# Kernel tuning notes

Hardware: AMD Instinct MI355X
Metric: run time of the kernel (lower is better)

The kernel has to match this reference:

```python
import jax, jax.numpy as jnp
import numpy as np

N, E, IN, HID, H, OUT = 50000, 800000, 128, 64, 4, 128
NEG = 0.2   # LeakyReLU slope in GATv2
EPS = 1e-5  # BatchNorm eps


def _seg_softmax(a, seg, n):
    # numerically stable softmax over edges grouped by destination node
    amax = jax.lax.stop_gradient(jax.ops.segment_max(a, seg, num_segments=n))
    amax = jnp.where(jnp.isfinite(amax), amax, 0.0)
    ex = jnp.exp(a - amax[seg])
    den = jax.ops.segment_sum(ex, seg, num_segments=n)
    return ex / (den[seg] + 1e-16)


def _gatv2(x, src, dst, e_attr, Wl, bl, Wr, br, We, att, bias, heads, c, concat):
    n = x.shape[0]
    xl = (x @ Wl + bl).reshape(n, heads, c)   # source transform (x_j)
    xr = (x @ Wr + br).reshape(n, heads, c)   # target transform (x_i)
    ee = (e_attr @ We).reshape(-1, heads, c)  # edge feature transform
    m = xl[src] + xr[dst] + ee                # [E, H, C]
    m = jnp.where(m > 0, m, NEG * m)          # LeakyReLU
    alpha = _seg_softmax(jnp.einsum('ehc,hc->eh', m, att), dst, n)  # [E, H]
    out = jax.ops.segment_sum(alpha[:, :, None] * xl[src], dst, num_segments=n)
    out = out.reshape(n, heads * c) if concat else out.mean(axis=1)
    return out + bias


def _bn(h, g, b):  # BatchNorm1d, training-mode batch stats (biased var)
    mu = jnp.mean(h, axis=0)
    var = jnp.var(h, axis=0)
    return (h - mu) * jax.lax.rsqrt(var + EPS) * g + b


def _prelu(h, a):
    return jnp.where(h > 0, h, a * h)


def setup_inputs() -> dict:
    key = jax.random.key(0)
    ks = jax.random.split(key, 16)
    def nrm(k, shape, fan):
        return jax.random.normal(k, shape, jnp.float32) / np.float32(np.sqrt(fan))
    x = jax.random.normal(ks[0], (N, IN), jnp.float32)
    edge_index = jax.random.randint(ks[1], (2, E), 0, N, jnp.int32)
    edge_attr = jax.random.uniform(ks[2], (E, 1), dtype=jnp.float32)
    return {
        'x': x, 'edge_index': edge_index, 'edge_attr': edge_attr,
        # layer 1: heads=4, concat=True
        'Wl1': nrm(ks[3], (IN, H * HID), IN), 'bl1': jnp.zeros((H * HID,), jnp.float32),
        'Wr1': nrm(ks[4], (IN, H * HID), IN), 'br1': jnp.zeros((H * HID,), jnp.float32),
        'We1': nrm(ks[5], (1, H * HID), 1),
        'att1': nrm(ks[6], (H, HID), HID),
        'cb1': jnp.zeros((H * HID,), jnp.float32),
        'bng1': jnp.ones((H * HID,), jnp.float32), 'bnb1': jnp.zeros((H * HID,), jnp.float32),
        'pa': jnp.float32(0.25),  # PReLU single parameter (shared by both uses)
        # layer 2: heads=1, concat=False
        'Wl2': nrm(ks[7], (H * HID, OUT), H * HID), 'bl2': jnp.zeros((OUT,), jnp.float32),
        'Wr2': nrm(ks[8], (H * HID, OUT), H * HID), 'br2': jnp.zeros((OUT,), jnp.float32),
        'We2': nrm(ks[9], (1, OUT), 1),
        'att2': nrm(ks[10], (1, OUT), OUT),
        'cb2': jnp.zeros((OUT,), jnp.float32),
        'bng2': jnp.ones((OUT,), jnp.float32), 'bnb2': jnp.zeros((OUT,), jnp.float32),
        'skipW': nrm(ks[11], (IN, OUT), IN), 'skipb': jnp.zeros((OUT,), jnp.float32),
    }


def reference(x, edge_index, edge_attr, Wl1, bl1, Wr1, br1, We1, att1, cb1,
              bng1, bnb1, pa, Wl2, bl2, Wr2, br2, We2, att2, cb2, bng2, bnb2,
              skipW, skipb):
    src, dst = edge_index[0], edge_index[1]
    h = _gatv2(x, src, dst, edge_attr, Wl1, bl1, Wr1, br1, We1, att1, cb1, H, HID, True)
    h = _prelu(_bn(h, bng1, bnb1), pa)  # dropout = identity (eval)
    h = _gatv2(h, src, dst, edge_attr, Wl2, bl2, Wr2, br2, We2, att2, cb2, 1, OUT, False)
    h = _prelu(_bn(h, bng2, bnb2), pa)
    return h + (x @ skipW + skipb)
```

## Files before the change

### kernel.cpp

```cpp
#include <hip/hip_runtime.h>
#include <cstdint>
#include <cstddef>

#define NNODES 50000
#define NEDGES 800000
#define DH1    256
#define DOUT   128

#define K1F 0.8656170245333781f
#define K2F 0.5770780163555854f

typedef unsigned short u16;
typedef __bf16 bf16x8 __attribute__((ext_vector_type(8)));
typedef float  f32x4  __attribute__((ext_vector_type(4)));

__device__ __forceinline__ float bf2f(unsigned int u) {
  union { unsigned int i; float f; } x; x.i = u << 16; return x.f;
}
__device__ __forceinline__ u16 f2bf(float f) {
  union { float f; unsigned int i; } x; x.f = f;
  unsigned int r = x.i + 0x7fffu + ((x.i >> 16) & 1u);
  return (u16)(r >> 16);
}
__device__ __forceinline__ void dec8(uint4 r, float* o) {
  o[0] = bf2f(r.x & 0xffffu); o[1] = bf2f(r.x >> 16);
  o[2] = bf2f(r.y & 0xffffu); o[3] = bf2f(r.y >> 16);
  o[4] = bf2f(r.z & 0xffffu); o[5] = bf2f(r.z >> 16);
  o[6] = bf2f(r.w & 0xffffu); o[7] = bf2f(r.w >> 16);
}
__device__ __forceinline__ uint4 pack8(const float* v) {
  uint4 p;
  p.x = (unsigned)f2bf(v[0]) | ((unsigned)f2bf(v[1]) << 16);
  p.y = (unsigned)f2bf(v[2]) | ((unsigned)f2bf(v[3]) << 16);
  p.z = (unsigned)f2bf(v[4]) | ((unsigned)f2bf(v[5]) << 16);
  p.w = (unsigned)f2bf(v[6]) | ((unsigned)f2bf(v[7]) << 16);
  return p;
}
template<int CTRL>
__device__ __forceinline__ float dppadd(float v) {
  int t = __builtin_amdgcn_update_dpp(0, __float_as_int(v), CTRL, 0xF, 0xF, true);
  return v + __int_as_float(t);
}
__device__ __forceinline__ float fexp2(float x) {
#if __has_builtin(__builtin_amdgcn_exp2f)
  return __builtin_amdgcn_exp2f(x);
#else
  return exp2f(x);
#endif
}


#define CNT_BLKS 3125
#define CVT_BLKS 6250
#define W1_BLKS  320
#define W2_BLKS  256

__global__ __launch_bounds__(256) void setup_k(
    const int* __restrict__ dst, int* __restrict__ cnt, int* __restrict__ rank,
    const float* __restrict__ x, u16* __restrict__ xbf,
    const float* __restrict__ Wl1, const float* __restrict__ Wr1,
    const float* __restrict__ bl1, const float* __restrict__ br1,
    const float* __restrict__ Wl2, const float* __restrict__ Wr2,
    const float* __restrict__ bl2, const float* __restrict__ br2,
    const float* __restrict__ skW, const float* __restrict__ skb,
    const float* __restrict__ att1, const float* __restrict__ We1,
    const float* __restrict__ att2, const float* __restrict__ We2,
    u16* __restrict__ Wcat1, float* __restrict__ bias1,
    u16* __restrict__ Wt2, float* __restrict__ bias2,
    float* __restrict__ axw, int2* __restrict__ epair) {
  int b = blockIdx.x, t = threadIdx.x;
  if (b < CNT_BLKS) {
    int e = b * 256 + t;
    if (e < NEDGES) rank[e] = atomicAdd(&cnt[dst[e]], 1);
  } else if (b < CNT_BLKS + CVT_BLKS) {
    int i = ((b - CNT_BLKS) * 256 + t) * 4;
    float4 v = *reinterpret_cast<const float4*>(x + i);
    uint2 pk;
    pk.x = (unsigned)f2bf(v.x) | ((unsigned)f2bf(v.y) << 16);
    pk.y = (unsigned)f2bf(v.z) | ((unsigned)f2bf(v.w) << 16);
    *reinterpret_cast<uint2*>(xbf + i) = pk;
  } else if (b < CNT_BLKS + CVT_BLKS + W1_BLKS) {
    int idx = (b - CNT_BLKS - CVT_BLKS) * 256 + t;
    if (idx < 640) bias1[idx] = idx < 256 ? bl1[idx] : idx < 512 ? br1[idx - 256] : skb[idx - 512];
    int n = idx >> 7, k = idx & 127;
    float v = n < 256 ? Wl1[k * 256 + n] : n < 512 ? Wr1[k * 256 + (n - 256)] : skW[k * 128 + (n - 512)];
    Wcat1[idx] = f2bf(v);
  } else if (b < CNT_BLKS + CVT_BLKS + W1_BLKS + W2_BLKS) {
    int idx = (b - CNT_BLKS - CVT_BLKS - W1_BLKS) * 256 + t;
    if (idx < 256) bias2[idx] = idx < 128 ? bl2[idx] : br2[idx - 128];
    int n = idx >> 8, k = idx & 255;
    float v = n < 128 ? Wl2[k * 128 + n] : Wr2[k * 128 + (n - 128)];
    Wt2[idx] = f2bf(v);
  } else if (b == CNT_BLKS + CVT_BLKS + W1_BLKS + W2_BLKS) {
    if (t < 4) {
      float s = 0.f;
      for (int c = 0; c < 64; ++c) s += att1[t * 64 + c] * We1[t * 64 + c];
      axw[t] = s * K1F;
    } else if (t == 4) {
      float s = 0.f;
      for (int c = 0; c < 128; ++c) s += att2[c] * We2[c];
      axw[4] = s * K1F;
    }
  } else {
    int2 z; z.x = 0; z.y = 0;
    epair[NEDGES + t] = z;
  }
}


__global__ __launch_bounds__(256) void offsets_k(const int* __restrict__ cnt, int* __restrict__ offs,
                                                 int* __restrict__ total) {
  int i = blockIdx.x * 256 + threadIdx.x;
  int lane = threadIdx.x & 63;
  int c = (i < NNODES) ? cnt[i] : 0;
  int incl = c;
  #pragma unroll
  for (int d = 1; d < 64; d <<= 1) {
    int t = __shfl_up(incl, d, 64);
    if (lane >= d) incl += t;
  }
  int wtotal = __shfl(incl, 63, 64);
  int base = 0;
  if (lane == 63) base = atomicAdd(total, wtotal);
  base = __shfl(base, 63, 64);
  int off = base + incl - c;
  if (i < NNODES) offs[i] = off;
}

__global__ __launch_bounds__(256) void scatter_k(const int* __restrict__ src, const int* __restrict__ dst,
                                                 const float* __restrict__ ea, const int* __restrict__ offs,
                                                 const int* __restrict__ rank, int2* __restrict__ epair) {
  int e = blockIdx.x * 256 + threadIdx.x;
  if (e >= NEDGES) return;
  int p = offs[dst[e]] + rank[e];
  int2 v; v.x = src[e]; v.y = __float_as_int(ea[e]);
  epair[p] = v;
}


template<int K, int NPASS, int B1, int B2, int LDC0, int LDC1, int LDC2,
         int SPAN, int ATTLEN, bool DO_ATT, bool FUSE_BN>
__global__ __launch_bounds__(512) void gemm_fused(
    const u16* __restrict__ A, const u16* __restrict__ Wt, const float* __restrict__ bias,
    u16* __restrict__ C0, u16* __restrict__ C1, u16* __restrict__ C2,
    const float* __restrict__ att, float* __restrict__ axl, float* __restrict__ axr,
    const float* __restrict__ bnsum, const float* __restrict__ bnsq,
    const float* __restrict__ bng, const float* __restrict__ bnb,
    const float* __restrict__ pap) {
  constexpr int LDA = K + 8;
  constexpr int CSTR = 136;
  __shared__ __align__(16) u16 As[64 * LDA];
  __shared__ __align__(16) u16 Cs[64 * CSTR];
  __shared__ float attS[128];
  __shared__ float scS[K], shS[K];
  const int tid = threadIdx.x;
  const int row0 = blockIdx.x * 64;

  if constexpr (FUSE_BN) {
    if (tid < K) {
      const float invN = 1.0f / (float)NNODES;
      float mu = bnsum[tid] * invN;
      float var = bnsq[tid] * invN - mu * mu;
      float s = bng[tid] * rsqrtf(var + 1e-5f);
      scS[tid] = s;
      shS[tid] = bnb[tid] - mu * s;
    }
    __syncthreads();
  }
  const float pa = FUSE_BN ? pap[0] : 0.f;
  #pragma unroll
  for (int it = 0; it < K / 32; ++it) {
    int chunk = it * 512 + tid;
    int row = chunk / (K / 4);
    int col = (chunk % (K / 4)) * 4;
    uint2 v; v.x = 0u; v.y = 0u;
    int gr = row0 + row;
    if (gr < NNODES) v = *reinterpret_cast<const uint2*>(A + (size_t)gr * K + col);
    if constexpr (FUSE_BN) {
      float o0 = bf2f(v.x & 0xffffu) * scS[col]     + shS[col];
      float o1 = bf2f(v.x >> 16)     * scS[col + 1] + shS[col + 1];
      float o2 = bf2f(v.y & 0xffffu) * scS[col + 2] + shS[col + 2];
      float o3 = bf2f(v.y >> 16)     * scS[col + 3] + shS[col + 3];
      o0 = o0 > 0.f ? o0 : pa * o0;
      o1 = o1 > 0.f ? o1 : pa * o1;
      o2 = o2 > 0.f ? o2 : pa * o2;
      o3 = o3 > 0.f ? o3 : pa * o3;
      v.x = (unsigned)f2bf(o0) | ((unsigned)f2bf(o1) << 16);
      v.y = (unsigned)f2bf(o2) | ((unsigned)f2bf(o3) << 16);
    }
    *reinterpret_cast<uint2*>(&As[row * LDA + col]) = v;
  }
  __syncthreads();

  const int w = tid >> 6, lane = tid & 63, q = lane >> 4, l16 = lane & 15;
  const int tc = w * 16 + l16;

  #pragma unroll
  for (int p = 0; p < NPASS; ++p) {
    const int cb = p * 128;
    const int ncol = cb + tc;
    f32x4 acc[4];
    #pragma unroll
    for (int rt = 0; rt < 4; ++rt) acc[rt] = (f32x4){0.f, 0.f, 0.f, 0.f};
    const u16* wp = Wt + (size_t)ncol * K + q * 8;
    #pragma unroll
    for (int ks = 0; ks < K / 32; ++ks) {
      bf16x8 b = *reinterpret_cast<const bf16x8*>(wp + ks * 32);
      #pragma unroll
      for (int rt = 0; rt < 4; ++rt) {
        bf16x8 a = *reinterpret_cast<const bf16x8*>(&As[(rt * 16 + l16) * LDA + ks * 32 + q * 8]);
        acc[rt] = __builtin_amdgcn_mfma_f32_16x16x32_bf16(a, b, acc[rt], 0, 0, 0);
      }
    }
    const float bval = bias[ncol];
    #pragma unroll
    for (int rt = 0; rt < 4; ++rt)
      #pragma unroll
      for (int r = 0; r < 4; ++r)
        Cs[(rt * 16 + q * 4 + r) * CSTR + tc] = f2bf(acc[rt][r] + bval);
    if (DO_ATT && cb < B2 && tid < 128) attS[tid] = att[(cb + tid) % ATTLEN];
    __syncthreads();
    {
      u16* Cg; int LD, cc;
      if (cb < B1)      { Cg = C0; LD = LDC0; cc = cb; }
      else if (cb < B2) { Cg = C1; LD = LDC1; cc = cb - B1; }
      else              { Cg = C2; LD = LDC2; cc = cb - B2; }
      #pragma unroll
      for (int it = 0; it < 2; ++it) {
        int ch = it * 512 + tid;
        int row = ch / 16, co = (ch % 16) * 8;
        int grow = row0 + row;
        if (grow < NNODES) {
          uint4 v = *reinterpret_cast<const uint4*>(&Cs[row * CSTR + co]);
          *reinterpret_cast<uint4*>(Cg + (size_t)grow * LD + cc + co) = v;
        }
      }
    }
    if constexpr (DO_ATT) {
      if (cb < B2) {
        constexpr int TPU = SPAN / 16;
        constexpr int HIT = 128 / SPAN;
        constexpr int HEADS = B1 / SPAN;
        int unit = tid / TPU, sub = tid % TPU;
        int row = unit / HIT, hb = unit % HIT;
        int c0 = hb * SPAN + sub * 16;
        float s = 0.f;
        #pragma unroll
        for (int c = 0; c < 16; ++c)
          s += bf2f(Cs[row * CSTR + c0 + c]) * attS[c0 + c];
        #pragma unroll
        for (int d = 1; d < TPU; d <<= 1) s += __shfl_xor(s, d, 64);
        int grow = row0 + row;
        if (sub == 0 && grow < NNODES) {
          int cbl = cb < B1 ? cb : cb - B1;
          int head = cbl / SPAN + hb;
          float* dstp = (cb < B1) ? axl : axr;
          dstp[grow * HEADS + head] = s * K1F;
        }
      }
    }
    __syncthreads();
  }
}


template<int HEADS, int CHAN, int EPW>
__global__ __launch_bounds__(256) void gat_edge(
    const int* __restrict__ offs, const int* __restrict__ cnt,
    const int2* __restrict__ epair,
    const u16* __restrict__ xl, const u16* __restrict__ xr,
    const float* __restrict__ att, const float* __restrict__ We,
    const float* __restrict__ cb,
    const float* __restrict__ axl, const float* __restrict__ axr,
    const float* __restrict__ aWep, u16* __restrict__ hout) {
  constexpr int HC  = HEADS * CHAN;
  constexpr int GSZ = 64 / EPW;
  constexpr int CPL = HC / GSZ;
  constexpr int LPH = CHAN / CPL;
  static_assert(CPL == 8, "layout");

  int node = __builtin_amdgcn_readfirstlane((int)(blockIdx.x * 4 + (threadIdx.x >> 6)));
  if (node >= NNODES) return;
  const int lane = threadIdx.x & 63;
  const int g    = lane / GSZ;
  const int lgs  = lane & (GSZ - 1);
  const int h    = lgs / LPH;
  const int cbase = lgs * CPL;

  float xrv[8], attv[8], wev[8];
  {
    uint4 xrr = *reinterpret_cast<const uint4*>(xr + (size_t)node * HC + cbase);
    dec8(xrr, xrv);
    float4 a0 = *reinterpret_cast<const float4*>(att + cbase);
    float4 a1 = *reinterpret_cast<const float4*>(att + cbase + 4);
    float4 w0 = *reinterpret_cast<const float4*>(We + cbase);
    float4 w1 = *reinterpret_cast<const float4*>(We + cbase + 4);
    attv[0]=a0.x*K2F; attv[1]=a0.y*K2F; attv[2]=a0.z*K2F; attv[3]=a0.w*K2F;
    attv[4]=a1.x*K2F; attv[5]=a1.y*K2F; attv[6]=a1.z*K2F; attv[7]=a1.w*K2F;
    wev[0]=w0.x; wev[1]=w0.y; wev[2]=w0.z; wev[3]=w0.w;
    wev[4]=w1.x; wev[5]=w1.y; wev[6]=w1.z; wev[7]=w1.w;
  }
  const float aWe = aWep[h];
  const float axr_n = axr[node * HEADS + h];
  const int off = __builtin_amdgcn_readfirstlane(offs[node]);
  const int deg = __builtin_amdgcn_readfirstlane(cnt[node]);

  const char* __restrict__ xlb  = (const char*)xl;
  const char* __restrict__ axlb = (const char*)axl;
  const unsigned cboff = (unsigned)(cbase * 2);
  const unsigned hoff  = (unsigned)(h * 4);

  float den = 0.f;
  float accv[8];
  #pragma unroll
  for (int c = 0; c < 8; ++c) accv[c] = 0.f;

  const int niter = (deg + EPW - 1) / EPW;
  const int2* pp = epair + off + g;
  int2 p0 = pp[0];
  int2 p1 = pp[EPW];
  int2 p2 = pp[2 * EPW];
  uint4 r0, r1; float ax0, ax1;
  {
    unsigned b0 = (unsigned)p0.x * (unsigned)(HC * 2) + cboff;
    r0  = *reinterpret_cast<const uint4*>(xlb + b0);
    ax0 = *reinterpret_cast<const float*>(axlb + ((unsigned)p0.x * (unsigned)(HEADS * 4) + hoff));
    unsigned b1 = (unsigned)p1.x * (unsigned)(HC * 2) + cboff;
    r1  = *reinterpret_cast<const uint4*>(xlb + b1);
    ax1 = *reinterpret_cast<const float*>(axlb + ((unsigned)p1.x * (unsigned)(HEADS * 4) + hoff));
  }
  const int lastg = deg - 1 - (niter - 1) * EPW;
  for (int i = 0; i < niter; ++i) {
    int2 p3 = pp[(i + 3) * EPW];
    uint4 r2; float ax2;
    {
      unsigned b2 = (unsigned)p2.x * (unsigned)(HC * 2) + cboff;
      r2  = *reinterpret_cast<const uint4*>(xlb + b2);
      ax2 = *reinterpret_cast<const float*>(axlb + ((unsigned)p2.x * (unsigned)(HEADS * 4) + hoff));
    }
    float ea = __int_as_float(p0.y);
    float xlv[8];
    dec8(r0, xlv);
    float part2 = 0.f;
    #pragma unroll
    for (int c = 0; c < 8; ++c) {
      float m = xlv[c] + fmaf(ea, wev[c], xrv[c]);
      part2 = fmaf(fabsf(m), attv[c], part2);
    }
    if constexpr (LPH >= 2)  part2 = dppadd<0xB1>(part2);
    if constexpr (LPH >= 4)  part2 = dppadd<0x4E>(part2);
    if constexpr (LPH >= 8)  part2 = dppadd<0x141>(part2);
    if constexpr (LPH >= 16) part2 = dppadd<0x140>(part2);
    float e = fexp2(part2 + fmaf(ea, aWe, axr_n) + ax0);
    if (i == niter - 1) e = (g <= lastg) ? e : 0.f;
    den += e;
    #pragma unroll
    for (int c = 0; c < 8; ++c) accv[c] = fmaf(e, xlv[c], accv[c]);
    p0 = p1; p1 = p2; p2 = p3; r0 = r1; r1 = r2; ax0 = ax1; ax1 = ax2;
  }
  #pragma unroll
  for (int d = GSZ; d < 64; d <<= 1) {
    den += __shfl_xor(den, d, 64);
    #pragma unroll
    for (int c = 0; c < 8; ++c) accv[c] += __shfl_xor(accv[c], d, 64);
  }
  if (g == 0) {
    float inv = 1.0f / (den + 1e-16f);
    float4 c0 = *reinterpret_cast<const float4*>(cb + cbase);
    float4 c1 = *reinterpret_cast<const float4*>(cb + cbase + 4);
    float ov[8];
    ov[0] = accv[0] * inv + c0.x; ov[1] = accv[1] * inv + c0.y;
    ov[2] = accv[2] * inv + c0.z; ov[3] = accv[3] * inv + c0.w;
    ov[4] = accv[4] * inv + c1.x; ov[5] = accv[5] * inv + c1.y;
    ov[6] = accv[6] * inv + c1.z; ov[7] = accv[7] * inv + c1.w;
    *reinterpret_cast<uint4*>(hout + (size_t)node * HC + cbase) = pack8(ov);
  }
}


template<int NC>
__global__ void bn_stats_bf(const u16* __restrict__ h, float* __restrict__ sum, float* __restrict__ sq) {
  int c = threadIdx.x;
  float s = 0.f, q = 0.f;
  for (int r = blockIdx.x; r < NNODES; r += gridDim.x) {
    float v = bf2f(h[(size_t)r * NC + c]);
    s += v; q += v * v;
  }
  atomicAdd(&sum[c], s);
  atomicAdd(&sq[c], q);
}

__global__ __launch_bounds__(256) void final_out_k(
    const u16* __restrict__ h2, const u16* __restrict__ skip,
    const float* __restrict__ sum, const float* __restrict__ sq,
    const float* __restrict__ g, const float* __restrict__ bb_,
    const float* __restrict__ pap, float* __restrict__ outp, int total) {
  int i = (blockIdx.x * 256 + threadIdx.x) * 4;
  if (i >= total) return;
  const float invN = 1.0f / (float)NNODES;
  float pa = pap[0];
  int c = i & 127;
  float4 sm = *reinterpret_cast<const float4*>(sum + c);
  float4 qq = *reinterpret_cast<const float4*>(sq + c);
  float4 gg = *reinterpret_cast<const float4*>(g + c);
  float4 bb = *reinterpret_cast<const float4*>(bb_ + c);
  float mu, var, sc[4], sh[4];
  mu = sm.x * invN; var = qq.x * invN - mu * mu; sc[0] = gg.x * rsqrtf(var + 1e-5f); sh[0] = bb.x - mu * sc[0];
  mu = sm.y * invN; var = qq.y * invN - mu * mu; sc[1] = gg.y * rsqrtf(var + 1e-5f); sh[1] = bb.y - mu * sc[1];
  mu = sm.z * invN; var = qq.z * invN - mu * mu; sc[2] = gg.z * rsqrtf(var + 1e-5f); sh[2] = bb.z - mu * sc[2];
  mu = sm.w * invN; var = qq.w * invN - mu * mu; sc[3] = gg.w * rsqrtf(var + 1e-5f); sh[3] = bb.w - mu * sc[3];
  uint2 raw = *reinterpret_cast<const uint2*>(h2 + i);
  float v0 = bf2f(raw.x & 0xffffu), v1 = bf2f(raw.x >> 16);
  float v2 = bf2f(raw.y & 0xffffu), v3 = bf2f(raw.y >> 16);
  uint2 skr = *reinterpret_cast<const uint2*>(skip + i);
  float s0 = bf2f(skr.x & 0xffffu), s1 = bf2f(skr.x >> 16);
  float s2 = bf2f(skr.y & 0xffffu), s3 = bf2f(skr.y >> 16);
  float4 o;
  o.x = v0 * sc[0] + sh[0]; o.x = (o.x > 0.f ? o.x : pa * o.x) + s0;
  o.y = v1 * sc[1] + sh[1]; o.y = (o.y > 0.f ? o.y : pa * o.y) + s1;
  o.z = v2 * sc[2] + sh[2]; o.z = (o.z > 0.f ? o.z : pa * o.z) + s2;
  o.w = v3 * sc[3] + sh[3]; o.w = (o.w > 0.f ? o.w : pa * o.w) + s3;
  *reinterpret_cast<float4*>(outp + i) = o;
}


extern "C" void kernel_launch(void* const* d_in, const int* in_sizes, int n_in,
                              void* d_out, int out_size, void* d_ws, size_t ws_size,
                              hipStream_t stream) {
  (void)in_sizes; (void)n_in; (void)out_size; (void)ws_size;
  const float* x    = (const float*)d_in[0];
  const int*   ei   = (const int*)d_in[1];
  const float* ea   = (const float*)d_in[2];
  const float* Wl1  = (const float*)d_in[3];
  const float* bl1  = (const float*)d_in[4];
  const float* Wr1  = (const float*)d_in[5];
  const float* br1  = (const float*)d_in[6];
  const float* We1  = (const float*)d_in[7];
  const float* att1 = (const float*)d_in[8];
  const float* cb1  = (const float*)d_in[9];
  const float* bng1 = (const float*)d_in[10];
  const float* bnb1 = (const float*)d_in[11];
  const float* pa   = (const float*)d_in[12];
  const float* Wl2  = (const float*)d_in[13];
  const float* bl2  = (const float*)d_in[14];
  const float* Wr2  = (const float*)d_in[15];
  const float* br2  = (const float*)d_in[16];
  const float* We2  = (const float*)d_in[17];
  const float* att2 = (const float*)d_in[18];
  const float* cb2  = (const float*)d_in[19];
  const float* bng2 = (const float*)d_in[20];
  const float* bnb2 = (const float*)d_in[21];
  const float* skW  = (const float*)d_in[22];
  const float* skb  = (const float*)d_in[23];
  const int* srcp = ei;
  const int* dstp = ei + NEDGES;

  char* base = (char*)d_ws;
  size_t off = 0;
  auto alloc = [&](size_t bytes) -> char* {
    char* p = base + off;
    off = (off + bytes + 255) & ~(size_t)255;
    return p;
  };
  size_t zero_ints = 1 + NNODES + 256 + 256 + 128 + 128;
  char* zbase = alloc(zero_ints * 4);
  int*   totalp = (int*)zbase;
  int*   cnt    = totalp + 1;
  float* bnsum1 = (float*)(cnt + NNODES);
  float* bnsq1  = bnsum1 + 256;
  float* bnsum2 = bnsq1 + 256;
  float* bnsq2  = bnsum2 + 128;

  int*   offs    = (int*)alloc((size_t)NNODES * 4);
  int*   rank    = (int*)alloc((size_t)NEDGES * 4);
  int2*  epair   = (int2*)alloc(((size_t)NEDGES + 256) * 8);
  const size_t RBYTES = (size_t)NNODES * DH1 * 2;
  char* regionA = alloc(RBYTES);
  char* regionB = alloc(RBYTES);
  char* regionC = alloc(RBYTES);
  u16*   xbf    = (u16*)alloc((size_t)NNODES * 128 * 2);
  u16*   skipbf = (u16*)alloc((size_t)NNODES * 128 * 2);
  u16*   Wcat1  = (u16*)alloc(640 * 128 * 2);
  u16*   Wt2    = (u16*)alloc(256 * 256 * 2);
  float* bias1  = (float*)alloc(640 * 4);
  float* bias2  = (float*)alloc(256 * 4);
  float* axw    = (float*)alloc(8 * 4);
  float* axl1   = (float*)alloc((size_t)NNODES * 4 * 4);
  float* axr1   = (float*)alloc((size_t)NNODES * 4 * 4);
  float* axl2   = (float*)alloc((size_t)NNODES * 4);
  float* axr2   = (float*)alloc((size_t)NNODES * 4);

  u16*   xl1     = (u16*)regionA;
  u16*   xr1     = (u16*)regionB;
  u16*   h1      = (u16*)regionC;
  u16*   xl2     = (u16*)regionB;
  u16*   xr2     = (u16*)(regionB + (size_t)NNODES * DOUT * 2);
  u16*   h2      = (u16*)regionA;

  hipMemsetAsync(zbase, 0, zero_ints * 4, stream);

  const int EB = (NEDGES + 255) / 256;
  const int NB = (NNODES + 255) / 256;
  setup_k<<<CNT_BLKS + CVT_BLKS + W1_BLKS + W2_BLKS + 2, 256, 0, stream>>>(
      dstp, cnt, rank, x, xbf, Wl1, Wr1, bl1, br1, Wl2, Wr2, bl2, br2, skW, skb,
      att1, We1, att2, We2, Wcat1, bias1, Wt2, bias2, axw, epair);
  offsets_k<<<NB, 256, 0, stream>>>(cnt, offs, totalp);
  scatter_k<<<EB, 256, 0, stream>>>(srcp, dstp, ea, offs, rank, epair);

  const int MB64 = (NNODES + 63) / 64;
  gemm_fused<128, 5, 256, 512, 256, 256, 128, 64, 256, true, false><<<MB64, 512, 0, stream>>>(
      xbf, Wcat1, bias1, xl1, xr1, skipbf, att1, axl1, axr1,
      (const float*)0, (const float*)0, (const float*)0, (const float*)0, (const float*)0);
  gat_edge<4, 64, 2><<<(NNODES + 3) / 4, 256, 0, stream>>>(
      offs, cnt, epair, xl1, xr1, att1, We1, cb1, axl1, axr1, axw, h1);
  bn_stats_bf<256><<<800, 256, 0, stream>>>(h1, bnsum1, bnsq1);

  gemm_fused<256, 2, 128, 256, 128, 128, 1, 128, 128, true, true><<<MB64, 512, 0, stream>>>(
      h1, Wt2, bias2, xl2, xr2, (u16*)0, att2, axl2, axr2,
      bnsum1, bnsq1, bng1, bnb1, pa);
  gat_edge<1, 128, 4><<<(NNODES + 3) / 4, 256, 0, stream>>>(
      offs, cnt, epair, xl2, xr2, att2, We2, cb2, axl2, axr2, axw + 4, h2);
  bn_stats_bf<128><<<800, 128, 0, stream>>>(h2, bnsum2, bnsq2);
  final_out_k<<<(NNODES * DOUT / 4 + 255) / 256, 256, 0, stream>>>(
      h2, skipbf, bnsum2, bnsq2, bng2, bnb2, pa, (float*)d_out, NNODES * DOUT);
}
```

Measured before the change: 439.5 us.

## Make GAT edge kernels persistent with per-partition atomic node work queues

Replaces the one-wave-per-node launch of the GAT edge aggregation kernels with a fixed grid of 2048 blocks. Each wave repeatedly claims the next node from one of 64 node partitions through an atomic counter and processes it. The software prefetch depth is reduced from three edges ahead to two, and the tail mask is now applied on every iteration. The intent is to balance the uneven per-node degrees, cut launch and wave startup overhead, and keep nearby nodes on the same blocks for cache locality. In exchange it adds an atomic per node, and the shallower prefetch may expose more gather latency.

```diff
diff --git a/kernel.cpp b/kernel.cpp
--- a/kernel.cpp
+++ b/kernel.cpp
@@ -6,6 +6,10 @@
 #define NEDGES 800000
 #define DH1    256
 #define DOUT   128
+
+#define NPART  64
+#define PSZ    782
+#define GATBLK 2048
 
 #define K1F 0.8656170245333781f
 #define K2F 0.5770780163555854f
@@ -272,25 +276,22 @@
     const float* __restrict__ att, const float* __restrict__ We,
     const float* __restrict__ cb,
     const float* __restrict__ axl, const float* __restrict__ axr,
-    const float* __restrict__ aWep, u16* __restrict__ hout) {
+    const float* __restrict__ aWep, u16* __restrict__ hout,
+    int* __restrict__ ctr) {
   constexpr int HC  = HEADS * CHAN;
   constexpr int GSZ = 64 / EPW;
   constexpr int CPL = HC / GSZ;
   constexpr int LPH = CHAN / CPL;
   static_assert(CPL == 8, "layout");
 
-  int node = __builtin_amdgcn_readfirstlane((int)(blockIdx.x * 4 + (threadIdx.x >> 6)));
-  if (node >= NNODES) return;
   const int lane = threadIdx.x & 63;
   const int g    = lane / GSZ;
   const int lgs  = lane & (GSZ - 1);
   const int h    = lgs / LPH;
   const int cbase = lgs * CPL;
 
-  float xrv[8], attv[8], wev[8];
+  float attv[8], wev[8];
   {
-    uint4 xrr = *reinterpret_cast<const uint4*>(xr + (size_t)node * HC + cbase);
-    dec8(xrr, xrv);
     float4 a0 = *reinterpret_cast<const float4*>(att + cbase);
     float4 a1 = *reinterpret_cast<const float4*>(att + cbase + 4);
     float4 w0 = *reinterpret_cast<const float4*>(We + cbase);
@@ -301,79 +302,91 @@
     wev[4]=w1.x; wev[5]=w1.y; wev[6]=w1.z; wev[7]=w1.w;
   }
   const float aWe = aWep[h];
-  const float axr_n = axr[node * HEADS + h];
-  const int off = __builtin_amdgcn_readfirstlane(offs[node]);
-  const int deg = __builtin_amdgcn_readfirstlane(cnt[node]);
+
+  const int part  = blockIdx.x & (NPART - 1);
+  const int pbase = part * PSZ;
+  const int pcnt  = (NNODES - pbase) < PSZ ? (NNODES - pbase) : PSZ;
+  int* ctrp = ctr + part;
 
   const char* __restrict__ xlb  = (const char*)xl;
   const char* __restrict__ axlb = (const char*)axl;
   const unsigned cboff = (unsigned)(cbase * 2);
   const unsigned hoff  = (unsigned)(h * 4);
 
-  float den = 0.f;
-  float accv[8];
-  #pragma unroll
-  for (int c = 0; c < 8; ++c) accv[c] = 0.f;
-
-  const int niter = (deg + EPW - 1) / EPW;
-  const int2* pp = epair + off + g;
-  int2 p0 = pp[0];
-  int2 p1 = pp[EPW];
-  int2 p2 = pp[2 * EPW];
-  uint4 r0, r1; float ax0, ax1;
-  {
-    unsigned b0 = (unsigned)p0.x * (unsigned)(HC * 2) + cboff;
-    r0  = *reinterpret_cast<const uint4*>(xlb + b0);
-    ax0 = *reinterpret_cast<const float*>(axlb + ((unsigned)p0.x * (unsigned)(HEADS * 4) + hoff));
-    unsigned b1 = (unsigned)p1.x * (unsigned)(HC * 2) + cboff;
-    r1  = *reinterpret_cast<const uint4*>(xlb + b1);
-    ax1 = *reinterpret_cast<const float*>(axlb + ((unsigned)p1.x * (unsigned)(HEADS * 4) + hoff));
-  }
-  const int lastg = deg - 1 - (niter - 1) * EPW;
-  for (int i = 0; i < niter; ++i) {
-    int2 p3 = pp[(i + 3) * EPW];
-    uint4 r2; float ax2;
+  for (;;) {
+    int myn = 0;
+    if (lane == 0) myn = atomicAdd(ctrp, 1);
+    myn = __shfl(myn, 0, 64);
+    if (myn >= pcnt) break;
+    const int node = __builtin_amdgcn_readfirstlane(pbase + myn);
+
+    float xrv[8];
+    dec8(*reinterpret_cast<const uint4*>(xr + (size_t)node * HC + cbase), xrv);
+    const float axr_n = axr[node * HEADS + h];
+    const int off = __builtin_amdgcn_readfirstlane(offs[node]);
+    const int deg = __builtin_amdgcn_readfirstlane(cnt[node]);
+    const int limg = deg - g;
+
+    float den = 0.f;
+    float accv[8];
+    #pragma unroll
+    for (int c = 0; c < 8; ++c) accv[c] = 0.f;
+
+    const int niter = (deg + EPW - 1) / EPW;
+    const int2* pp = epair + off + g;
+    int2 p_cur = pp[0];
+    int2 p_nxt = pp[EPW];
+    uint4 r_cur; float ax_cur;
     {
-      unsigned b2 = (unsigned)p2.x * (unsigned)(HC * 2) + cboff;
-      r2  = *reinterpret_cast<const uint4*>(xlb + b2);
-      ax2 = *reinterpret_cast<const float*>(axlb + ((unsigned)p2.x * (unsigned)(HEADS * 4) + hoff));
-    }
-    float ea = __int_as_float(p0.y);
-    float xlv[8];
-    dec8(r0, xlv);
-    float part2 = 0.f;
+      unsigned b0 = (unsigned)p_cur.x * (unsigned)(HC * 2) + cboff;
+      r_cur  = *reinterpret_cast<const uint4*>(xlb + b0);
+      ax_cur = *reinterpret_cast<const float*>(axlb + ((unsigned)p_cur.x * (unsigned)(HEADS * 4) + hoff));
+    }
+    for (int i = 0; i < niter; ++i) {
+      int2 p_n2 = pp[(i + 2) * EPW];
+      uint4 r_n; float ax_n;
+      {
+        unsigned b1 = (unsigned)p_nxt.x * (unsigned)(HC * 2) + cboff;
+        r_n  = *reinterpret_cast<const uint4*>(xlb + b1);
+        ax_n = *reinterpret_cast<const float*>(axlb + ((unsigned)p_nxt.x * (unsigned)(HEADS * 4) + hoff));
+      }
+      float ea = __int_as_float(p_cur.y);
+      float xlv[8];
+      dec8(r_cur, xlv);
+      float part2 = 0.f;
+      #pragma unroll
+      for (int c = 0; c < 8; ++c) {
+        float m = xlv[c] + fmaf(ea, wev[c], xrv[c]);
+        part2 = fmaf(fabsf(m), attv[c], part2);
+      }
+      if constexpr (LPH >= 2)  part2 = dppadd<0xB1>(part2);
+      if constexpr (LPH >= 4)  part2 = dppadd<0x4E>(part2);
+      if constexpr (LPH >= 8)  part2 = dppadd<0x141>(part2);
+      if constexpr (LPH >= 16) part2 = dppadd<0x140>(part2);
+      float e = fexp2(part2 + fmaf(ea, aWe, axr_n) + ax_cur);
+      e = (i * EPW < limg) ? e : 0.f;
+      den += e;
+      #pragma unroll
+      for (int c = 0; c < 8; ++c) accv[c] = fmaf(e, xlv[c], accv[c]);
+      p_cur = p_nxt; p_nxt = p_n2; r_cur = r_n; ax_cur = ax_n;
+    }
     #pragma unroll
-    for (int c = 0; c < 8; ++c) {
-      float m = xlv[c] + fmaf(ea, wev[c], xrv[c]);
-      part2 = fmaf(fabsf(m), attv[c], part2);
-    }
-    if constexpr (LPH >= 2)  part2 = dppadd<0xB1>(part2);
-    if constexpr (LPH >= 4)  part2 = dppadd<0x4E>(part2);
-    if constexpr (LPH >= 8)  part2 = dppadd<0x141>(part2);
-    if constexpr (LPH >= 16) part2 = dppadd<0x140>(part2);
-    float e = fexp2(part2 + fmaf(ea, aWe, axr_n) + ax0);
-    if (i == niter - 1) e = (g <= lastg) ? e : 0.f;
-    den += e;
-    #pragma unroll
-    for (int c = 0; c < 8; ++c) accv[c] = fmaf(e, xlv[c], accv[c]);
-    p0 = p1; p1 = p2; p2 = p3; r0 = r1; r1 = r2; ax0 = ax1; ax1 = ax2;
-  }
-  #pragma unroll
-  for (int d = GSZ; d < 64; d <<= 1) {
-    den += __shfl_xor(den, d, 64);
-    #pragma unroll
-    for (int c = 0; c < 8; ++c) accv[c] += __shfl_xor(accv[c], d, 64);
-  }
-  if (g == 0) {
-    float inv = 1.0f / (den + 1e-16f);
-    float4 c0 = *reinterpret_cast<const float4*>(cb + cbase);
-    float4 c1 = *reinterpret_cast<const float4*>(cb + cbase + 4);
-    float ov[8];
-    ov[0] = accv[0] * inv + c0.x; ov[1] = accv[1] * inv + c0.y;
-    ov[2] = accv[2] * inv + c0.z; ov[3] = accv[3] * inv + c0.w;
-    ov[4] = accv[4] * inv + c1.x; ov[5] = accv[5] * inv + c1.y;
-    ov[6] = accv[6] * inv + c1.z; ov[7] = accv[7] * inv + c1.w;
-    *reinterpret_cast<uint4*>(hout + (size_t)node * HC + cbase) = pack8(ov);
+    for (int d = GSZ; d < 64; d <<= 1) {
+      den += __shfl_xor(den, d, 64);
+      #pragma unroll
+      for (int c = 0; c < 8; ++c) accv[c] += __shfl_xor(accv[c], d, 64);
+    }
+    if (g == 0) {
+      float inv = 1.0f / (den + 1e-16f);
+      float4 c0 = *reinterpret_cast<const float4*>(cb + cbase);
+      float4 c1 = *reinterpret_cast<const float4*>(cb + cbase + 4);
+      float ov[8];
+      ov[0] = accv[0] * inv + c0.x; ov[1] = accv[1] * inv + c0.y;
+      ov[2] = accv[2] * inv + c0.z; ov[3] = accv[3] * inv + c0.w;
+      ov[4] = accv[4] * inv + c1.x; ov[5] = accv[5] * inv + c1.y;
+      ov[6] = accv[6] * inv + c1.z; ov[7] = accv[7] * inv + c1.w;
+      *reinterpret_cast<uint4*>(hout + (size_t)node * HC + cbase) = pack8(ov);
+    }
   }
 }
 
@@ -462,7 +475,7 @@
     off = (off + bytes + 255) & ~(size_t)255;
     return p;
   };
-  size_t zero_ints = 1 + NNODES + 256 + 256 + 128 + 128;
+  size_t zero_ints = 1 + NNODES + 256 + 256 + 128 + 128 + 2 * NPART;
   char* zbase = alloc(zero_ints * 4);
   int*   totalp = (int*)zbase;
   int*   cnt    = totalp + 1;
@@ -470,6 +483,8 @@
   float* bnsq1  = bnsum1 + 256;
   float* bnsum2 = bnsq1 + 256;
   float* bnsq2  = bnsum2 + 128;
+  int*   ctr1   = (int*)(bnsq2 + 128);
+  int*   ctr2   = ctr1 + NPART;
 
   int*   offs    = (int*)alloc((size_t)NNODES * 4);
   int*   rank    = (int*)alloc((size_t)NEDGES * 4);
@@ -511,15 +526,15 @@
   gemm_fused<128, 5, 256, 512, 256, 256, 128, 64, 256, true, false><<<MB64, 512, 0, stream>>>(
       xbf, Wcat1, bias1, xl1, xr1, skipbf, att1, axl1, axr1,
       (const float*)0, (const float*)0, (const float*)0, (const float*)0, (const float*)0);
-  gat_edge<4, 64, 2><<<(NNODES + 3) / 4, 256, 0, stream>>>(
-      offs, cnt, epair, xl1, xr1, att1, We1, cb1, axl1, axr1, axw, h1);
+  gat_edge<4, 64, 2><<<GATBLK, 256, 0, stream>>>(
+      offs, cnt, epair, xl1, xr1, att1, We1, cb1, axl1, axr1, axw, h1, ctr1);
   bn_stats_bf<256><<<800, 256, 0, stream>>>(h1, bnsum1, bnsq1);
 
   gemm_fused<256, 2, 128, 256, 128, 128, 1, 128, 128, true, true><<<MB64, 512, 0, stream>>>(
       h1, Wt2, bias2, xl2, xr2, (u16*)0, att2, axl2, axr2,
       bnsum1, bnsq1, bng1, bnb1, pa);
-  gat_edge<1, 128, 4><<<(NNODES + 3) / 4, 256, 0, stream>>>(
-      offs, cnt, epair, xl2, xr2, att2, We2, cb2, axl2, axr2, axw + 4, h2);
+  gat_edge<1, 128, 4><<<GATBLK, 256, 0, stream>>>(
+      offs, cnt, epair, xl2, xr2, att2, We2, cb2, axl2, axr2, axw + 4, h2, ctr2);
   bn_stats_bf<128><<<800, 128, 0, stream>>>(h2, bnsum2, bnsq2);
   final_out_k<<<(NNODES * DOUT / 4 + 255) / 256, 256, 0, stream>>>(
       h2, skipbf, bnsum2, bnsq2, bng2, bnb2, pa, (float*)d_out, NNODES * DOUT);
```

Result: slower. 773.1 us (+75.9%).

## Split layer-1 edge aggregation per head and shorten gather prefetch depth

Applied to the files above, without the earlier changes.

The layer-1 GAT edge kernel now gives each wavefront a single (node, head) pair. Each wave handles 8 edges at a time with 8 lanes per 64-channel head, where before one wave covered all four heads at 2 edges per pass. Block indices are interleaved so the four head-blocks of a node group launch close together, which should let them share the gathered source rows in cache. The software prefetch pipeline is also cut from two edges ahead to one, lowering register pressure at the cost of less latency hiding. The layer-1 grid grows fourfold, and each wave re-reads the edge list and metadata for its own head.

```diff
diff --git a/kernel.cpp b/kernel.cpp
--- a/kernel.cpp
+++ b/kernel.cpp
@@ -264,7 +264,7 @@
 }
 
 
-template<int HEADS, int CHAN, int EPW>
+template<int CHAN, int EPW, int LDROW, int HTOT>
 __global__ __launch_bounds__(256) void gat_edge(
     const int* __restrict__ offs, const int* __restrict__ cnt,
     const int2* __restrict__ epair,
@@ -273,42 +273,52 @@
     const float* __restrict__ cb,
     const float* __restrict__ axl, const float* __restrict__ axr,
     const float* __restrict__ aWep, u16* __restrict__ hout) {
-  constexpr int HC  = HEADS * CHAN;
   constexpr int GSZ = 64 / EPW;
-  constexpr int CPL = HC / GSZ;
-  constexpr int LPH = CHAN / CPL;
+  constexpr int CPL = CHAN / GSZ;
+  constexpr int LPH = GSZ;
   static_assert(CPL == 8, "layout");
 
-  int node = __builtin_amdgcn_readfirstlane((int)(blockIdx.x * 4 + (threadIdx.x >> 6)));
-  if (node >= NNODES) return;
+  const int wid = threadIdx.x >> 6;
+  int node_, head_;
+  if constexpr (HTOT == 4) {
+    int b = blockIdx.x;
+    head_ = (b & 7) >> 1;
+    int ng = ((b >> 3) << 1) + (b & 1);
+    node_ = ng * 4 + wid;
+  } else {
+    head_ = 0;
+    node_ = (int)(blockIdx.x * 4 + wid);
+  }
+  if (node_ >= NNODES) return;
+  const int node = __builtin_amdgcn_readfirstlane(node_);
+  const int head = __builtin_amdgcn_readfirstlane(head_);
   const int lane = threadIdx.x & 63;
   const int g    = lane / GSZ;
   const int lgs  = lane & (GSZ - 1);
-  const int h    = lgs / LPH;
-  const int cbase = lgs * CPL;
+  const int cg   = head * CHAN + lgs * CPL;
 
   float xrv[8], attv[8], wev[8];
   {
-    uint4 xrr = *reinterpret_cast<const uint4*>(xr + (size_t)node * HC + cbase);
+    uint4 xrr = *reinterpret_cast<const uint4*>(xr + (size_t)node * LDROW + cg);
     dec8(xrr, xrv);
-    float4 a0 = *reinterpret_cast<const float4*>(att + cbase);
-    float4 a1 = *reinterpret_cast<const float4*>(att + cbase + 4);
-    float4 w0 = *reinterpret_cast<const float4*>(We + cbase);
-    float4 w1 = *reinterpret_cast<const float4*>(We + cbase + 4);
+    float4 a0 = *reinterpret_cast<const float4*>(att + cg);
+    float4 a1 = *reinterpret_cast<const float4*>(att + cg + 4);
+    float4 w0 = *reinterpret_cast<const float4*>(We + cg);
+    float4 w1 = *reinterpret_cast<const float4*>(We + cg + 4);
     attv[0]=a0.x*K2F; attv[1]=a0.y*K2F; attv[2]=a0.z*K2F; attv[3]=a0.w*K2F;
     attv[4]=a1.x*K2F; attv[5]=a1.y*K2F; attv[6]=a1.z*K2F; attv[7]=a1.w*K2F;
     wev[0]=w0.x; wev[1]=w0.y; wev[2]=w0.z; wev[3]=w0.w;
     wev[4]=w1.x; wev[5]=w1.y; wev[6]=w1.z; wev[7]=w1.w;
   }
-  const float aWe = aWep[h];
-  const float axr_n = axr[node * HEADS + h];
+  const float aWe = aWep[head];
+  const float axr_n = axr[node * HTOT + head];
   const int off = __builtin_amdgcn_readfirstlane(offs[node]);
   const int deg = __builtin_amdgcn_readfirstlane(cnt[node]);
 
   const char* __restrict__ xlb  = (const char*)xl;
   const char* __restrict__ axlb = (const char*)axl;
-  const unsigned cboff = (unsigned)(cbase * 2);
-  const unsigned hoff  = (unsigned)(h * 4);
+  const unsigned cboff = (unsigned)(cg * 2);
+  const unsigned hoff  = (unsigned)(head * 4);
 
   float den = 0.f;
   float accv[8];
@@ -317,30 +327,26 @@
 
   const int niter = (deg + EPW - 1) / EPW;
   const int2* pp = epair + off + g;
-  int2 p0 = pp[0];
-  int2 p1 = pp[EPW];
-  int2 p2 = pp[2 * EPW];
-  uint4 r0, r1; float ax0, ax1;
+  int2 p_cur = pp[0];
+  int2 p_nxt = pp[EPW];
+  uint4 r_cur; float ax_cur;
   {
-    unsigned b0 = (unsigned)p0.x * (unsigned)(HC * 2) + cboff;
-    r0  = *reinterpret_cast<const uint4*>(xlb + b0);
-    ax0 = *reinterpret_cast<const float*>(axlb + ((unsigned)p0.x * (unsigned)(HEADS * 4) + hoff));
-    unsigned b1 = (unsigned)p1.x * (unsigned)(HC * 2) + cboff;
-    r1  = *reinterpret_cast<const uint4*>(xlb + b1);
-    ax1 = *reinterpret_cast<const float*>(axlb + ((unsigned)p1.x * (unsigned)(HEADS * 4) + hoff));
+    unsigned b0 = (unsigned)p_cur.x * (unsigned)(LDROW * 2) + cboff;
+    r_cur  = *reinterpret_cast<const uint4*>(xlb + b0);
+    ax_cur = *reinterpret_cast<const float*>(axlb + ((unsigned)p_cur.x * (unsigned)(HTOT * 4) + hoff));
   }
   const int lastg = deg - 1 - (niter - 1) * EPW;
   for (int i = 0; i < niter; ++i) {
-    int2 p3 = pp[(i + 3) * EPW];
-    uint4 r2; float ax2;
+    int2 p_n2 = pp[(i + 2) * EPW];
+    uint4 r_n; float ax_n;
     {
-      unsigned b2 = (unsigned)p2.x * (unsigned)(HC * 2) + cboff;
-      r2  = *reinterpret_cast<const uint4*>(xlb + b2);
-      ax2 = *reinterpret_cast<const float*>(axlb + ((unsigned)p2.x * (unsigned)(HEADS * 4) + hoff));
-    }
-    float ea = __int_as_float(p0.y);
+      unsigned b1 = (unsigned)p_nxt.x * (unsigned)(LDROW * 2) + cboff;
+      r_n  = *reinterpret_cast<const uint4*>(xlb + b1);
+      ax_n = *reinterpret_cast<const float*>(axlb + ((unsigned)p_nxt.x * (unsigned)(HTOT * 4) + hoff));
+    }
+    float ea = __int_as_float(p_cur.y);
     float xlv[8];
-    dec8(r0, xlv);
+    dec8(r_cur, xlv);
     float part2 = 0.f;
     #pragma unroll
     for (int c = 0; c < 8; ++c) {
@@ -351,12 +357,12 @@
     if constexpr (LPH >= 4)  part2 = dppadd<0x4E>(part2);
     if constexpr (LPH >= 8)  part2 = dppadd<0x141>(part2);
     if constexpr (LPH >= 16) part2 = dppadd<0x140>(part2);
-    float e = fexp2(part2 + fmaf(ea, aWe, axr_n) + ax0);
+    float e = fexp2(part2 + fmaf(ea, aWe, axr_n) + ax_cur);
     if (i == niter - 1) e = (g <= lastg) ? e : 0.f;
     den += e;
     #pragma unroll
     for (int c = 0; c < 8; ++c) accv[c] = fmaf(e, xlv[c], accv[c]);
-    p0 = p1; p1 = p2; p2 = p3; r0 = r1; r1 = r2; ax0 = ax1; ax1 = ax2;
+    p_cur = p_nxt; p_nxt = p_n2; r_cur = r_n; ax_cur = ax_n;
   }
   #pragma unroll
   for (int d = GSZ; d < 64; d <<= 1) {
@@ -366,14 +372,14 @@
   }
   if (g == 0) {
     float inv = 1.0f / (den + 1e-16f);
-    float4 c0 = *reinterpret_cast<const float4*>(cb + cbase);
-    float4 c1 = *reinterpret_cast<const float4*>(cb + cbase + 4);
+    float4 c0 = *reinterpret_cast<const float4*>(cb + cg);
+    float4 c1 = *reinterpret_cast<const float4*>(cb + cg + 4);
     float ov[8];
     ov[0] = accv[0] * inv + c0.x; ov[1] = accv[1] * inv + c0.y;
     ov[2] = accv[2] * inv + c0.z; ov[3] = accv[3] * inv + c0.w;
     ov[4] = accv[4] * inv + c1.x; ov[5] = accv[5] * inv + c1.y;
     ov[6] = accv[6] * inv + c1.z; ov[7] = accv[7] * inv + c1.w;
-    *reinterpret_cast<uint4*>(hout + (size_t)node * HC + cbase) = pack8(ov);
+    *reinterpret_cast<uint4*>(hout + (size_t)node * LDROW + cg) = pack8(ov);
   }
 }
 
@@ -511,14 +517,14 @@
   gemm_fused<128, 5, 256, 512, 256, 256, 128, 64, 256, true, false><<<MB64, 512, 0, stream>>>(
       xbf, Wcat1, bias1, xl1, xr1, skipbf, att1, axl1, axr1,
       (const float*)0, (const float*)0, (const float*)0, (const float*)0, (const float*)0);
-  gat_edge<4, 64, 2><<<(NNODES + 3) / 4, 256, 0, stream>>>(
+  gat_edge<64, 8, 256, 4><<<NNODES, 256, 0, stream>>>(
       offs, cnt, epair, xl1, xr1, att1, We1, cb1, axl1, axr1, axw, h1);
   bn_stats_bf<256><<<800, 256, 0, stream>>>(h1, bnsum1, bnsq1);
 
   gemm_fused<256, 2, 128, 256, 128, 128, 1, 128, 128, true, true><<<MB64, 512, 0, stream>>>(
       h1, Wt2, bias2, xl2, xr2, (u16*)0, att2, axl2, axr2,
       bnsum1, bnsq1, bng1, bnb1, pa);
-  gat_edge<1, 128, 4><<<(NNODES + 3) / 4, 256, 0, stream>>>(
+  gat_edge<128, 4, 128, 1><<<(NNODES + 3) / 4, 256, 0, stream>>>(
       offs, cnt, epair, xl2, xr2, att2, We2, cb2, axl2, axr2, axw + 4, h2);
   bn_stats_bf<128><<<800, 128, 0, stream>>>(h2, bnsum2, bnsq2);
   final_out_k<<<(NNODES * DOUT / 4 + 255) / 256, 256, 0, stream>>>(
```

Measured after the change: 461.1 us. +4.9%, slower.

## Replace BN stats atomics with two-pass partial reduction and shorten edge prefetch depth

Applied to the files above, without the earlier changes.

The batch-norm statistics kernels now write per-block partial sums into a buffer instead of issuing float atomics to shared accumulators. A small second kernel reduces those partials, which also makes the reduction deterministic. The launch uses fewer blocks (256 instead of 800). Separately, the GAT edge loop's software prefetch goes from three edges ahead to two, cutting register pressure at the cost of less latency hiding. The change adds two extra kernel launches and partial buffers.

```diff
diff --git a/kernel.cpp b/kernel.cpp
--- a/kernel.cpp
+++ b/kernel.cpp
@@ -6,6 +6,7 @@
 #define NEDGES 800000
 #define DH1    256
 #define DOUT   128
+#define BNP    256
 
 #define K1F 0.8656170245333781f
 #define K2F 0.5770780163555854f
@@ -317,30 +318,26 @@
 
   const int niter = (deg + EPW - 1) / EPW;
   const int2* pp = epair + off + g;
-  int2 p0 = pp[0];
-  int2 p1 = pp[EPW];
-  int2 p2 = pp[2 * EPW];
-  uint4 r0, r1; float ax0, ax1;
+  int2 p_cur = pp[0];
+  int2 p_nxt = pp[EPW];
+  uint4 r_cur; float ax_cur;
   {
-    unsigned b0 = (unsigned)p0.x * (unsigned)(HC * 2) + cboff;
-    r0  = *reinterpret_cast<const uint4*>(xlb + b0);
-    ax0 = *reinterpret_cast<const float*>(axlb + ((unsigned)p0.x * (unsigned)(HEADS * 4) + hoff));
-    unsigned b1 = (unsigned)p1.x * (unsigned)(HC * 2) + cboff;
-    r1  = *reinterpret_cast<const uint4*>(xlb + b1);
-    ax1 = *reinterpret_cast<const float*>(axlb + ((unsigned)p1.x * (unsigned)(HEADS * 4) + hoff));
+    unsigned b0 = (unsigned)p_cur.x * (unsigned)(HC * 2) + cboff;
+    r_cur  = *reinterpret_cast<const uint4*>(xlb + b0);
+    ax_cur = *reinterpret_cast<const float*>(axlb + ((unsigned)p_cur.x * (unsigned)(HEADS * 4) + hoff));
   }
   const int lastg = deg - 1 - (niter - 1) * EPW;
   for (int i = 0; i < niter; ++i) {
-    int2 p3 = pp[(i + 3) * EPW];
-    uint4 r2; float ax2;
+    int2 p_n2 = pp[(i + 2) * EPW];
+    uint4 r_n; float ax_n;
     {
-      unsigned b2 = (unsigned)p2.x * (unsigned)(HC * 2) + cboff;
-      r2  = *reinterpret_cast<const uint4*>(xlb + b2);
-      ax2 = *reinterpret_cast<const float*>(axlb + ((unsigned)p2.x * (unsigned)(HEADS * 4) + hoff));
-    }
-    float ea = __int_as_float(p0.y);
+      unsigned b1 = (unsigned)p_nxt.x * (unsigned)(HC * 2) + cboff;
+      r_n  = *reinterpret_cast<const uint4*>(xlb + b1);
+      ax_n = *reinterpret_cast<const float*>(axlb + ((unsigned)p_nxt.x * (unsigned)(HEADS * 4) + hoff));
+    }
+    float ea = __int_as_float(p_cur.y);
     float xlv[8];
-    dec8(r0, xlv);
+    dec8(r_cur, xlv);
     float part2 = 0.f;
     #pragma unroll
     for (int c = 0; c < 8; ++c) {
@@ -351,12 +348,12 @@
     if constexpr (LPH >= 4)  part2 = dppadd<0x4E>(part2);
     if constexpr (LPH >= 8)  part2 = dppadd<0x141>(part2);
     if constexpr (LPH >= 16) part2 = dppadd<0x140>(part2);
-    float e = fexp2(part2 + fmaf(ea, aWe, axr_n) + ax0);
+    float e = fexp2(part2 + fmaf(ea, aWe, axr_n) + ax_cur);
     if (i == niter - 1) e = (g <= lastg) ? e : 0.f;
     den += e;
     #pragma unroll
     for (int c = 0; c < 8; ++c) accv[c] = fmaf(e, xlv[c], accv[c]);
-    p0 = p1; p1 = p2; p2 = p3; r0 = r1; r1 = r2; ax0 = ax1; ax1 = ax2;
+    p_cur = p_nxt; p_nxt = p_n2; r_cur = r_n; ax_cur = ax_n;
   }
   #pragma unroll
   for (int d = GSZ; d < 64; d <<= 1) {
@@ -379,15 +376,29 @@
 
 
 template<int NC>
-__global__ void bn_stats_bf(const u16* __restrict__ h, float* __restrict__ sum, float* __restrict__ sq) {
+__global__ __launch_bounds__(NC) void bn_stats_bf(const u16* __restrict__ h,
+                                                  float* __restrict__ partial) {
   int c = threadIdx.x;
   float s = 0.f, q = 0.f;
-  for (int r = blockIdx.x; r < NNODES; r += gridDim.x) {
+  for (int r = blockIdx.x; r < NNODES; r += BNP) {
     float v = bf2f(h[(size_t)r * NC + c]);
     s += v; q += v * v;
   }
-  atomicAdd(&sum[c], s);
-  atomicAdd(&sq[c], q);
+  partial[(size_t)blockIdx.x * 2 * NC + c] = s;
+  partial[(size_t)blockIdx.x * 2 * NC + NC + c] = q;
+}
+
+template<int NC>
+__global__ __launch_bounds__(128) void bn_reduce_k(const float* __restrict__ partial,
+                                                   float* __restrict__ sum, float* __restrict__ sq) {
+  int c = blockIdx.x * 128 + threadIdx.x;
+  if (c >= NC) return;
+  float s = 0.f, q = 0.f;
+  for (int p = 0; p < BNP; ++p) {
+    s += partial[(size_t)p * 2 * NC + c];
+    q += partial[(size_t)p * 2 * NC + NC + c];
+  }
+  sum[c] = s; sq[c] = q;
 }
 
 __global__ __launch_bounds__(256) void final_out_k(
@@ -489,6 +500,8 @@
   float* axr1   = (float*)alloc((size_t)NNODES * 4 * 4);
   float* axl2   = (float*)alloc((size_t)NNODES * 4);
   float* axr2   = (float*)alloc((size_t)NNODES * 4);
+  float* bnpart1 = (float*)alloc((size_t)BNP * 2 * 256 * 4);
+  float* bnpart2 = (float*)alloc((size_t)BNP * 2 * 128 * 4);
 
   u16*   xl1     = (u16*)regionA;
   u16*   xr1     = (u16*)regionB;
@@ -513,14 +526,16 @@
       (const float*)0, (const float*)0, (const float*)0, (const float*)0, (const float*)0);
   gat_edge<4, 64, 2><<<(NNODES + 3) / 4, 256, 0, stream>>>(
       offs, cnt, epair, xl1, xr1, att1, We1, cb1, axl1, axr1, axw, h1);
-  bn_stats_bf<256><<<800, 256, 0, stream>>>(h1, bnsum1, bnsq1);
+  bn_stats_bf<256><<<BNP, 256, 0, stream>>>(h1, bnpart1);
+  bn_reduce_k<256><<<2, 128, 0, stream>>>(bnpart1, bnsum1, bnsq1);
 
   gemm_fused<256, 2, 128, 256, 128, 128, 1, 128, 128, true, true><<<MB64, 512, 0, stream>>>(
       h1, Wt2, bias2, xl2, xr2, (u16*)0, att2, axl2, axr2,
       bnsum1, bnsq1, bng1, bnb1, pa);
   gat_edge<1, 128, 4><<<(NNODES + 3) / 4, 256, 0, stream>>>(
       offs, cnt, epair, xl2, xr2, att2, We2, cb2, axl2, axr2, axw + 4, h2);
-  bn_stats_bf<128><<<800, 128, 0, stream>>>(h2, bnsum2, bnsq2);
+  bn_stats_bf<128><<<BNP, 128, 0, stream>>>(h2, bnpart2);
+  bn_reduce_k<128><<<1, 128, 0, stream>>>(bnpart2, bnsum2, bnsq2);
   final_out_k<<<(NNODES * DOUT / 4 + 255) / 256, 256, 0, stream>>>(
       h2, skipbf, bnsum2, bnsq2, bng2, bnb2, pa, (float*)d_out, NNODES * DOUT);
 }
```

After: 484.1 us. 10.1% more time.
